# Kernel optimization log

Hardware: AMD Instinct MI355X
Metric: run time of the kernel (lower is better)

Reference implementation:

```python
import jax, jax.numpy as jnp
import numpy as np

B, H, N, D, RPE = 2, 8, 4096, 64, 64
LAYERS = 3


def _rms(x):
    # SimpleRMSNorm: x / sqrt(mean(x^2) + eps), no learned scale
    return x / jnp.sqrt(jnp.mean(x * x, axis=-1, keepdims=True) + 1e-8)


def setup_inputs() -> dict:
    key = jax.random.key(0)
    ks = jax.random.split(key, 7)
    s = 1.0 / np.sqrt(RPE)
    return {
        "x": jax.random.normal(ks[0], (B, H, N, D), dtype=jnp.float32),
        "w_in": jax.random.normal(ks[1], (1, RPE), dtype=jnp.float32) * 0.5,
        "b_in": jax.random.normal(ks[2], (RPE,), dtype=jnp.float32) * 0.02,
        "w_hid": jax.random.normal(ks[3], (LAYERS, RPE, RPE), dtype=jnp.float32) * s,
        "b_hid": jax.random.normal(ks[4], (LAYERS, RPE), dtype=jnp.float32) * 0.02,
        "w_out": jax.random.normal(ks[5], (RPE, H * D), dtype=jnp.float32) * s,
        "b_out": jax.random.normal(ks[6], (H * D,), dtype=jnp.float32) * 0.02,
    }


def reference(x, w_in, b_in, w_hid, b_hid, w_out, b_out):
    n = x.shape[-2]
    dt = x.dtype

    def rpe(idx):  # idx: (m, 1) relative-position features
        h = idx @ w_in + b_in  # (m, RPE)
        for i in range(LAYERS):  # non-residual: x = layer(x)
            h = jax.nn.relu(_rms(h)) @ w_hid[i] + b_hid[i]
        h = jax.nn.relu(_rms(h)) @ w_out + b_out  # (m, H*D)
        return h.reshape(-1, H, D).transpose(1, 0, 2)  # (H, m, D)

    zero_idx = jnp.ones((1, 1), dt)
    pos_idx = (1.0 / jnp.arange(2, n + 1, dtype=dt)).reshape(n - 1, 1)
    neg_idx = (-1.0 / jnp.arange(n, 1, -1, dtype=dt)).reshape(n - 1, 1)

    zero_k = rpe(zero_idx)  # (H, 1, D); used for both T[0] slots like the torch code
    a = jnp.concatenate([zero_k, rpe(pos_idx), zero_k, rpe(neg_idx)], axis=1)  # (H, 2n, D)
    # act_type='none' -> identity activation on a

    # Toeplitz matvec as circular conv of length 2n via FFT
    y = jnp.fft.rfft(x, 2 * n, axis=-2)          # (B, H, n+1, D) complex
    v = jnp.fft.rfft(a, 2 * n, axis=-2)[None]    # (1, H, n+1, D) complex
    out = jnp.fft.irfft(v * y, 2 * n, axis=-2)[:, :, :n, :]
    return out.astype(dt)
```

## Files before the change

kernel.cpp:

```cpp
#include <hip/hip_runtime.h>

#define N_SEQ 4096
#define N_FFT 8192
#define LAYERS 3
#define FT 512
#define PIDX(i) ((i) + ((i) >> 5))

template<int M>
__device__ inline void pass16_fwd(float* re, float* im, int tid)
{
    const int Q = M >> 4;
    const int j = tid & (Q - 1);
    const int G = tid / Q;
    const int base = G * M + j;
    const float KR[4] = {1.f, 0.9238795325f, 0.7071067812f, 0.3826834324f};
    const float KI[4] = {0.f, -0.3826834324f, -0.7071067812f, -0.9238795325f};
    float xr[4][4], xi[4][4];
#pragma unroll
    for (int a = 0; a < 4; ++a)
#pragma unroll
        for (int b = 0; b < 4; ++b) {
            int idx = PIDX(base + a * (M >> 2) + b * Q);
            xr[a][b] = re[idx]; xi[a][b] = im[idx];
        }
    float cj, sj;
    __sincosf(-6.283185307179586f / (float)M * (float)j, &sj, &cj);
#pragma unroll
    for (int b = 0; b < 4; ++b) {
        float c1 = cj * KR[b] - sj * KI[b];
        float s1 = cj * KI[b] + sj * KR[b];
        float c2 = c1 * c1 - s1 * s1, s2 = 2.f * c1 * s1;
        float c3 = c2 * c1 - s2 * s1, s3 = c2 * s1 + s2 * c1;
        float ar = xr[0][b] + xr[2][b], ai = xi[0][b] + xi[2][b];
        float br = xr[0][b] - xr[2][b], bi = xi[0][b] - xi[2][b];
        float cr = xr[1][b] + xr[3][b], ci = xi[1][b] + xi[3][b];
        float dr = xi[1][b] - xi[3][b], di = -(xr[1][b] - xr[3][b]);
        xr[0][b] = ar + cr;               xi[0][b] = ai + ci;
        float t1r = br + dr, t1i = bi + di;
        xr[1][b] = t1r * c1 - t1i * s1;   xi[1][b] = t1r * s1 + t1i * c1;
        float t2r = ar - cr, t2i = ai - ci;
        xr[2][b] = t2r * c2 - t2i * s2;   xi[2][b] = t2r * s2 + t2i * c2;
        float t3r = br - dr, t3i = bi - di;
        xr[3][b] = t3r * c3 - t3i * s3;   xi[3][b] = t3r * s3 + t3i * c3;
    }
    {
        float e1c = cj * cj - sj * sj, e1s = 2.f * cj * sj;
        float c1 = e1c * e1c - e1s * e1s, s1 = 2.f * e1c * e1s;
        float c2 = c1 * c1 - s1 * s1, s2 = 2.f * c1 * s1;
        float c3 = c2 * c1 - s2 * s1, s3 = c2 * s1 + s2 * c1;
#pragma unroll
        for (int a = 0; a < 4; ++a) {
            float ar = xr[a][0] + xr[a][2], ai = xi[a][0] + xi[a][2];
            float br = xr[a][0] - xr[a][2], bi = xi[a][0] - xi[a][2];
            float cr = xr[a][1] + xr[a][3], ci = xi[a][1] + xi[a][3];
            float dr = xi[a][1] - xi[a][3], di = -(xr[a][1] - xr[a][3]);
            xr[a][0] = ar + cr;               xi[a][0] = ai + ci;
            float t1r = br + dr, t1i = bi + di;
            xr[a][1] = t1r * c1 - t1i * s1;   xi[a][1] = t1r * s1 + t1i * c1;
            float t2r = ar - cr, t2i = ai - ci;
            xr[a][2] = t2r * c2 - t2i * s2;   xi[a][2] = t2r * s2 + t2i * c2;
            float t3r = br - dr, t3i = bi - di;
            xr[a][3] = t3r * c3 - t3i * s3;   xi[a][3] = t3r * s3 + t3i * c3;
        }
    }
#pragma unroll
    for (int a = 0; a < 4; ++a)
#pragma unroll
        for (int b = 0; b < 4; ++b) {
            int idx = PIDX(base + a * (M >> 2) + b * Q);
            re[idx] = xr[a][b]; im[idx] = xi[a][b];
        }
}

template<int M>
__device__ inline void pass16_inv(float* re, float* im, int tid)
{
    const int Q = M >> 4;
    const int j = tid & (Q - 1);
    const int G = tid / Q;
    const int base = G * M + j;
    const float KR[4] = {1.f, 0.9238795325f, 0.7071067812f, 0.3826834324f};
    const float KI[4] = {0.f, 0.3826834324f, 0.7071067812f, 0.9238795325f};
    float xr[4][4], xi[4][4];
#pragma unroll
    for (int a = 0; a < 4; ++a)
#pragma unroll
        for (int b = 0; b < 4; ++b) {
            int idx = PIDX(base + a * (M >> 2) + b * Q);
            xr[a][b] = re[idx]; xi[a][b] = im[idx];
        }
    float cj, sj;
    __sincosf(6.283185307179586f / (float)M * (float)j, &sj, &cj);
    {
        float e1c = cj * cj - sj * sj, e1s = 2.f * cj * sj;
        float c1 = e1c * e1c - e1s * e1s, s1 = 2.f * e1c * e1s;
        float c2 = c1 * c1 - s1 * s1, s2 = 2.f * c1 * s1;
        float c3 = c2 * c1 - s2 * s1, s3 = c2 * s1 + s2 * c1;
#pragma unroll
        for (int a = 0; a < 4; ++a) {
            float t0r = xr[a][0], t0i = xi[a][0];
            float t1r = xr[a][1] * c1 - xi[a][1] * s1, t1i = xr[a][1] * s1 + xi[a][1] * c1;
            float t2r = xr[a][2] * c2 - xi[a][2] * s2, t2i = xr[a][2] * s2 + xi[a][2] * c2;
            float t3r = xr[a][3] * c3 - xi[a][3] * s3, t3i = xr[a][3] * s3 + xi[a][3] * c3;
            float pr = t0r + t2r, pi = t0i + t2i;
            float qr = t0r - t2r, qi = t0i - t2i;
            float rr = t1r + t3r, ri = t1i + t3i;
            float sr = -(t1i - t3i), si = t1r - t3r;
            xr[a][0] = pr + rr; xi[a][0] = pi + ri;
            xr[a][1] = qr + sr; xi[a][1] = qi + si;
            xr[a][2] = pr - rr; xi[a][2] = pi - ri;
            xr[a][3] = qr - sr; xi[a][3] = qi - si;
        }
    }
#pragma unroll
    for (int b = 0; b < 4; ++b) {
        float c1 = cj * KR[b] - sj * KI[b];
        float s1 = cj * KI[b] + sj * KR[b];
        float c2 = c1 * c1 - s1 * s1, s2 = 2.f * c1 * s1;
        float c3 = c2 * c1 - s2 * s1, s3 = c2 * s1 + s2 * c1;
        float t0r = xr[0][b], t0i = xi[0][b];
        float t1r = xr[1][b] * c1 - xi[1][b] * s1, t1i = xr[1][b] * s1 + xi[1][b] * c1;
        float t2r = xr[2][b] * c2 - xi[2][b] * s2, t2i = xr[2][b] * s2 + xi[2][b] * c2;
        float t3r = xr[3][b] * c3 - xi[3][b] * s3, t3i = xr[3][b] * s3 + xi[3][b] * c3;
        float pr = t0r + t2r, pi = t0i + t2i;
        float qr = t0r - t2r, qi = t0i - t2i;
        float rr = t1r + t3r, ri = t1i + t3i;
        float sr = -(t1i - t3i), si = t1r - t3r;
        xr[0][b] = pr + rr; xi[0][b] = pi + ri;
        xr[1][b] = qr + sr; xi[1][b] = qi + si;
        xr[2][b] = pr - rr; xi[2][b] = pi - ri;
        xr[3][b] = qr - sr; xi[3][b] = qi - si;
    }
#pragma unroll
    for (int a = 0; a < 4; ++a)
#pragma unroll
        for (int b = 0; b < 4; ++b) {
            int idx = PIDX(base + a * (M >> 2) + b * Q);
            re[idx] = xr[a][b]; im[idx] = xi[a][b];
        }
}

__device__ inline void fwd8(float* zr, float* zi, int o)
{
    const float R = 0.70710678118654752f;
    {
        float ar = zr[o] + zr[o+4], ai = zi[o] + zi[o+4];
        float br = zr[o] - zr[o+4], bi = zi[o] - zi[o+4];
        float cr = zr[o+2] + zr[o+6], ci = zi[o+2] + zi[o+6];
        float dr = zi[o+2] - zi[o+6], di = -(zr[o+2] - zr[o+6]);
        zr[o]   = ar + cr; zi[o]   = ai + ci;
        zr[o+2] = br + dr; zi[o+2] = bi + di;
        zr[o+4] = ar - cr; zi[o+4] = ai - ci;
        zr[o+6] = br - dr; zi[o+6] = bi - di;
    }
    {
        float ar = zr[o+1] + zr[o+5], ai = zi[o+1] + zi[o+5];
        float br = zr[o+1] - zr[o+5], bi = zi[o+1] - zi[o+5];
        float cr = zr[o+3] + zr[o+7], ci = zi[o+3] + zi[o+7];
        float dr = zi[o+3] - zi[o+7], di = -(zr[o+3] - zr[o+7]);
        zr[o+1] = ar + cr; zi[o+1] = ai + ci;
        float t1r = br + dr, t1i = bi + di;
        zr[o+3] = R * (t1r + t1i); zi[o+3] = R * (t1i - t1r);
        float t2r = ar - cr, t2i = ai - ci;
        zr[o+5] = t2i;  zi[o+5] = -t2r;
        float t3r = br - dr, t3i = bi - di;
        zr[o+7] = R * (t3i - t3r); zi[o+7] = -R * (t3r + t3i);
    }
#pragma unroll
    for (int p = 0; p < 8; p += 2) {
        float ur = zr[o+p], ui = zi[o+p], vr = zr[o+p+1], vi = zi[o+p+1];
        zr[o+p]   = ur + vr; zi[o+p]   = ui + vi;
        zr[o+p+1] = ur - vr; zi[o+p+1] = ui - vi;
    }
}

__device__ inline void inv8(float* zr, float* zi, int o)
{
    const float R = 0.70710678118654752f;
#pragma unroll
    for (int p = 0; p < 8; p += 2) {
        float ur = zr[o+p], ui = zi[o+p], vr = zr[o+p+1], vi = zi[o+p+1];
        zr[o+p]   = ur + vr; zi[o+p]   = ui + vi;
        zr[o+p+1] = ur - vr; zi[o+p+1] = ui - vi;
    }
    {
        float t0r = zr[o],   t0i = zi[o];
        float t1r = zr[o+2], t1i = zi[o+2];
        float t2r = zr[o+4], t2i = zi[o+4];
        float t3r = zr[o+6], t3i = zi[o+6];
        float pr = t0r + t2r, pi = t0i + t2i;
        float qr = t0r - t2r, qi = t0i - t2i;
        float rr = t1r + t3r, ri = t1i + t3i;
        float sr = -(t1i - t3i), si = t1r - t3r;
        zr[o]   = pr + rr; zi[o]   = pi + ri;
        zr[o+2] = qr + sr; zi[o+2] = qi + si;
        zr[o+4] = pr - rr; zi[o+4] = pi - ri;
        zr[o+6] = qr - sr; zi[o+6] = qi - si;
    }
    {
        float t0r = zr[o+1], t0i = zi[o+1];
        float yr = zr[o+3], yi = zi[o+3];
        float t1r = R * (yr - yi), t1i = R * (yr + yi);
        yr = zr[o+5]; yi = zi[o+5];
        float t2r = -yi, t2i = yr;
        yr = zr[o+7]; yi = zi[o+7];
        float t3r = -R * (yr + yi), t3i = R * (yr - yi);
        float pr = t0r + t2r, pi = t0i + t2i;
        float qr = t0r - t2r, qi = t0i - t2i;
        float rr = t1r + t3r, ri = t1i + t3i;
        float sr = -(t1i - t3i), si = t1r - t3r;
        zr[o+1] = pr + rr; zi[o+1] = pi + ri;
        zr[o+3] = qr + sr; zi[o+3] = qi + si;
        zr[o+5] = pr - rr; zi[o+5] = pi - ri;
        zr[o+7] = qr - sr; zi[o+7] = qi - si;
    }
}

__global__ __launch_bounds__(256) void prep_kernel(
    const float* __restrict__ x,
    const float* __restrict__ w_in, const float* __restrict__ b_in,
    const float* __restrict__ w_hid, const float* __restrict__ b_hid,
    const float* __restrict__ w_out, const float* __restrict__ b_out,
    float* __restrict__ a_t, float2* __restrict__ xt2)
{
    __shared__ __align__(16) char smem[33536];
    const int tid = threadIdx.x;

    if (blockIdx.x >= 256) {
        float (*t0)[65] = (float (*)[65])smem;
        float (*t1)[65] = (float (*)[65])(smem + 16640);
        int bb = blockIdx.x - 256;
        int h = bb >> 6;
        int nb = bb & 63;
        int lx = tid & 63;
        int ly = tid >> 6;
        const float* s0 = x + ((size_t)h * N_SEQ + nb * 64) * 64;
        const float* s1 = x + ((size_t)(8 + h) * N_SEQ + nb * 64) * 64;
        for (int r = ly; r < 64; r += 4) {
            t0[r][lx] = s0[r * 64 + lx];
            t1[r][lx] = s1[r * 64 + lx];
        }
        __syncthreads();
        for (int r = ly; r < 64; r += 4) {
            float2* dst = xt2 + (size_t)(h * 64 + r) * N_SEQ + nb * 64;
            dst[lx] = make_float2(t0[lx][r], t1[lx][r]);
        }
        return;
    }

    float4* wl       = (float4*)smem;
    float (*ubuf)[65] = (float (*)[65])(smem + 16384);
    float (*sums)[9]  = (float (*)[9])(smem + 24704);
    const int p   = tid & 31;
    const int oct = tid >> 5;
    const int pos = blockIdx.x * 32 + p;

    float v;
    if (pos == 0 || pos == N_SEQ) v = 1.0f;
    else if (pos < N_SEQ)         v = 1.0f / (float)(pos + 1);
    else                          v = -1.0f / (float)(2 * N_SEQ + 1 - pos);

    float h[8];
#pragma unroll
    for (int i = 0; i < 8; ++i) {
        int f = oct * 8 + i;
        h[i] = v * w_in[f] + b_in[f];
    }
    for (int L = 0; L < LAYERS; ++L) {
        const float4* wsrc = (const float4*)(w_hid + L * 4096);
#pragma unroll
        for (int i = 0; i < 4; ++i) wl[i * 256 + tid] = wsrc[i * 256 + tid];
        float s = 0.f;
#pragma unroll
        for (int i = 0; i < 8; ++i) s += h[i] * h[i];
        sums[p][oct] = s;
        __syncthreads();
        float tot = 0.f;
#pragma unroll
        for (int g = 0; g < 8; ++g) tot += sums[p][g];
        float r = rsqrtf(tot * (1.f / 64.f) + 1e-8f);
#pragma unroll
        for (int i = 0; i < 8; ++i)
            ubuf[p][oct * 8 + i] = fmaxf(h[i] * r, 0.f);
        __syncthreads();
        float acc[8];
#pragma unroll
        for (int i = 0; i < 8; ++i) acc[i] = b_hid[L * 64 + oct * 8 + i];
#pragma unroll 4
        for (int j = 0; j < 64; ++j) {
            float uj = ubuf[p][j];
            float4 w0 = wl[j * 16 + oct * 2];
            float4 w1 = wl[j * 16 + oct * 2 + 1];
            acc[0] = fmaf(uj, w0.x, acc[0]); acc[1] = fmaf(uj, w0.y, acc[1]);
            acc[2] = fmaf(uj, w0.z, acc[2]); acc[3] = fmaf(uj, w0.w, acc[3]);
            acc[4] = fmaf(uj, w1.x, acc[4]); acc[5] = fmaf(uj, w1.y, acc[5]);
            acc[6] = fmaf(uj, w1.z, acc[6]); acc[7] = fmaf(uj, w1.w, acc[7]);
        }
#pragma unroll
        for (int i = 0; i < 8; ++i) h[i] = acc[i];
        __syncthreads();
    }
    {
        float s = 0.f;
#pragma unroll
        for (int i = 0; i < 8; ++i) s += h[i] * h[i];
        sums[p][oct] = s;
        __syncthreads();
        float tot = 0.f;
#pragma unroll
        for (int g = 0; g < 8; ++g) tot += sums[p][g];
        float r = rsqrtf(tot * (1.f / 64.f) + 1e-8f);
#pragma unroll
        for (int i = 0; i < 8; ++i)
            ubuf[p][oct * 8 + i] = fmaxf(h[i] * r, 0.f);
        __syncthreads();
    }
    for (int c = 0; c < 8; ++c) {
        float4 wreg[4];
#pragma unroll
        for (int cc = 0; cc < 4; ++cc) {
            int i4 = cc * 256 + tid;
            int j = i4 >> 4, q = i4 & 15;
            wreg[cc] = *(const float4*)(w_out + j * 512 + c * 64 + q * 4);
        }
        __syncthreads();
#pragma unroll
        for (int cc = 0; cc < 4; ++cc) wl[cc * 256 + tid] = wreg[cc];
        __syncthreads();
        float acc[8];
#pragma unroll
        for (int i = 0; i < 8; ++i) acc[i] = b_out[c * 64 + oct * 8 + i];
#pragma unroll 4
        for (int j = 0; j < 64; ++j) {
            float uj = ubuf[p][j];
            float4 w0 = wl[j * 16 + oct * 2];
            float4 w1 = wl[j * 16 + oct * 2 + 1];
            acc[0] = fmaf(uj, w0.x, acc[0]); acc[1] = fmaf(uj, w0.y, acc[1]);
            acc[2] = fmaf(uj, w0.z, acc[2]); acc[3] = fmaf(uj, w0.w, acc[3]);
            acc[4] = fmaf(uj, w1.x, acc[4]); acc[5] = fmaf(uj, w1.y, acc[5]);
            acc[6] = fmaf(uj, w1.z, acc[6]); acc[7] = fmaf(uj, w1.w, acc[7]);
        }
#pragma unroll
        for (int i = 0; i < 8; ++i)
            a_t[(size_t)(c * 64 + oct * 8 + i) * N_FFT + pos] = acc[i];
    }
}

__global__ __launch_bounds__(FT, 4) void conv_kernel(const float* __restrict__ a_t,
                                                     const float2* __restrict__ xt2,
                                                     float2* __restrict__ out_t2)
{
    __shared__ float re[8448];
    __shared__ float im[8448];
    const int tid = threadIdx.x;
    const int hd = blockIdx.x;
    const float JR = 0.9238795325f;
    const float JI = -0.3826834324f;

    {
        const float* src = a_t + (size_t)hd * N_FFT;
        float ck, sk;
        __sincosf(-6.283185307179586f / 8192.f * (float)tid, &sk, &ck);
#pragma unroll
        for (int pp = 0; pp < 4; ++pp) {
            int k = pp * FT + tid;
            float x0 = src[k], x1 = src[k + 2048], x2 = src[k + 4096], x3 = src[k + 6144];
            float ar = x0 + x2, br = x0 - x2;
            float cr = x1 + x3, e = x1 - x3;
            re[PIDX(k)] = ar + cr; im[PIDX(k)] = 0.f;
            float c1 = ck, s1 = sk;
            float c2 = c1 * c1 - s1 * s1, s2 = 2.f * c1 * s1;
            float c3 = c2 * c1 - s2 * s1, s3 = c2 * s1 + s2 * c1;
            re[PIDX(k + 2048)] = br * c1 + e * s1;  im[PIDX(k + 2048)] = br * s1 - e * c1;
            float t2r = ar - cr;
            re[PIDX(k + 4096)] = t2r * c2;          im[PIDX(k + 4096)] = t2r * s2;
            re[PIDX(k + 6144)] = br * c3 - e * s3;  im[PIDX(k + 6144)] = br * s3 + e * c3;
            float tc = ck * JR - sk * JI; sk = ck * JI + sk * JR; ck = tc;
        }
    }
    __syncthreads();
    pass16_fwd<2048>(re, im, tid);
    __syncthreads();
    pass16_fwd<128>(re, im, tid);
    __syncthreads();
    float afr[16], afi[16];
    {
        const int base = tid * 16;
        float zr[16], zi[16];
#pragma unroll
        for (int c = 0; c < 16; ++c) { int idx = PIDX(base + c); zr[c] = re[idx]; zi[c] = im[idx]; }
        fwd8(zr, zi, 0); fwd8(zr, zi, 8);
        const float inv = 1.0f / (float)N_FFT;
#pragma unroll
        for (int c = 0; c < 16; ++c) { afr[c] = zr[c] * inv; afi[c] = zi[c] * inv; }
    }
    __syncthreads();
    {
        const float2* src = xt2 + (size_t)hd * N_SEQ;
        float ck, sk;
        __sincosf(-6.283185307179586f / 8192.f * (float)tid, &sk, &ck);
#pragma unroll
        for (int pp = 0; pp < 4; ++pp) {
            int k = pp * FT + tid;
            float2 z0 = src[k], z1 = src[k + 2048];
            float ar = z0.x, ai = z0.y;
            float cr = z1.x, ci = z1.y;
            float dr = z1.y, di = -z1.x;
            re[PIDX(k)] = ar + cr; im[PIDX(k)] = ai + ci;
            float c1 = ck, s1 = sk;
            float c2 = c1 * c1 - s1 * s1, s2 = 2.f * c1 * s1;
            float c3 = c2 * c1 - s2 * s1, s3 = c2 * s1 + s2 * c1;
            float t1r = ar + dr, t1i = ai + di;
            re[PIDX(k + 2048)] = t1r * c1 - t1i * s1; im[PIDX(k + 2048)] = t1r * s1 + t1i * c1;
            float t2r = ar - cr, t2i = ai - ci;
            re[PIDX(k + 4096)] = t2r * c2 - t2i * s2; im[PIDX(k + 4096)] = t2r * s2 + t2i * c2;
            float t3r = ar - dr, t3i = ai - di;
            re[PIDX(k + 6144)] = t3r * c3 - t3i * s3; im[PIDX(k + 6144)] = t3r * s3 + t3i * c3;
            float tc = ck * JR - sk * JI; sk = ck * JI + sk * JR; ck = tc;
        }
    }
    __syncthreads();
    pass16_fwd<2048>(re, im, tid);
    __syncthreads();
    pass16_fwd<128>(re, im, tid);
    __syncthreads();
    {
        const int base = tid * 16;
        float zr[16], zi[16];
#pragma unroll
        for (int c = 0; c < 16; ++c) { int idx = PIDX(base + c); zr[c] = re[idx]; zi[c] = im[idx]; }
        fwd8(zr, zi, 0); fwd8(zr, zi, 8);
#pragma unroll
        for (int c = 0; c < 16; ++c) {
            float xr = zr[c], xi_ = zi[c];
            zr[c] = xr * afr[c] - xi_ * afi[c];
            zi[c] = xr * afi[c] + xi_ * afr[c];
        }
        inv8(zr, zi, 0); inv8(zr, zi, 8);
#pragma unroll
        for (int c = 0; c < 16; ++c) { int idx = PIDX(base + c); re[idx] = zr[c]; im[idx] = zi[c]; }
    }
    __syncthreads();
    pass16_inv<128>(re, im, tid);
    __syncthreads();
    pass16_inv<2048>(re, im, tid);
    __syncthreads();
    {
        float2* dst = out_t2 + (size_t)hd * N_SEQ;
        float ck, sk;
        __sincosf(6.283185307179586f / 8192.f * (float)tid, &sk, &ck);
        const float JcR = 0.9238795325f, JcI = 0.3826834324f;
#pragma unroll
        for (int pp = 0; pp < 4; ++pp) {
            int k = pp * FT + tid;
            float c1 = ck, s1 = sk;
            float c2 = c1 * c1 - s1 * s1, s2 = 2.f * c1 * s1;
            float c3 = c2 * c1 - s2 * s1, s3 = c2 * s1 + s2 * c1;
            float t0r = re[PIDX(k)],        t0i = im[PIDX(k)];
            float y1r = re[PIDX(k + 2048)], y1i = im[PIDX(k + 2048)];
            float y2r = re[PIDX(k + 4096)], y2i = im[PIDX(k + 4096)];
            float y3r = re[PIDX(k + 6144)], y3i = im[PIDX(k + 6144)];
            float t1r = y1r * c1 - y1i * s1, t1i = y1r * s1 + y1i * c1;
            float t2r = y2r * c2 - y2i * s2, t2i = y2r * s2 + y2i * c2;
            float t3r = y3r * c3 - y3i * s3, t3i = y3r * s3 + y3i * c3;
            float pr = t0r + t2r, pi = t0i + t2i;
            float qr = t0r - t2r, qi = t0i - t2i;
            float rr = t1r + t3r, ri = t1i + t3i;
            float sr = -(t1i - t3i), si = t1r - t3r;
            dst[k]        = make_float2(pr + rr, pi + ri);
            dst[k + 2048] = make_float2(qr + sr, qi + si);
            float tc = ck * JcR - sk * JcI; sk = ck * JcI + sk * JcR; ck = tc;
        }
    }
}

__global__ __launch_bounds__(256) void transpose_o_kernel(const float2* __restrict__ out_t2,
                                                          float* __restrict__ out)
{
    __shared__ float t0[64][65];
    __shared__ float t1[64][65];
    int h = blockIdx.x >> 6;
    int nb = blockIdx.x & 63;
    int lx = threadIdx.x & 63;
    int ly = threadIdx.x >> 6;
    for (int r = ly; r < 64; r += 4) {
        float2 v = out_t2[(size_t)(h * 64 + r) * N_SEQ + nb * 64 + lx];
        t0[r][lx] = v.x;
        t1[r][lx] = v.y;
    }
    __syncthreads();
    float* d0 = out + ((size_t)h * N_SEQ + nb * 64) * 64;
    float* d1 = out + ((size_t)(8 + h) * N_SEQ + nb * 64) * 64;
    for (int r = ly; r < 64; r += 4) {
        d0[r * 64 + lx] = t0[lx][r];
        d1[r * 64 + lx] = t1[lx][r];
    }
}

extern "C" void kernel_launch(void* const* d_in, const int* in_sizes, int n_in,
                              void* d_out, int out_size, void* d_ws, size_t ws_size,
                              hipStream_t stream)
{
    const float* x     = (const float*)d_in[0];
    const float* w_in  = (const float*)d_in[1];
    const float* b_in  = (const float*)d_in[2];
    const float* w_hid = (const float*)d_in[3];
    const float* b_hid = (const float*)d_in[4];
    const float* w_out = (const float*)d_in[5];
    const float* b_out = (const float*)d_in[6];
    float* out = (float*)d_out;

    char* ws = (char*)d_ws;
    float2* xt2    = (float2*)ws;
    float*  a_t    = (float*)(ws + (size_t)16 * 1024 * 1024);
    float2* out_t2 = (float2*)(ws + (size_t)32 * 1024 * 1024);

    prep_kernel<<<768, 256, 0, stream>>>(x, w_in, b_in, w_hid, b_hid, w_out, b_out,
                                         a_t, xt2);
    conv_kernel<<<512, FT, 0, stream>>>(a_t, xt2, out_t2);
    transpose_o_kernel<<<512, 256, 0, stream>>>(out_t2, out);
}
```

Before: 169.7 us.

## Widen prep blocks to 512 threads, relax conv launch bounds, defer FFT scaling

The prep kernel now runs 512-thread blocks handling 64 positions each, halving the MLP block count and loading each weight tile with fewer, wider per-thread copies. The transpose blocks use 8 row groups per pass. The conv kernel's launch bounds drop from 4 to 2 blocks per SM to give the compiler more registers, and the 1/N scale moves from the kernel-spectrum setup into the pointwise product. The relaxed bound may cost occupancy, and the larger MLP blocks reduce parallelism across the grid.

```diff
diff --git a/kernel.cpp b/kernel.cpp
--- a/kernel.cpp
+++ b/kernel.cpp
@@ -216,44 +216,44 @@
     }
 }
 
-__global__ __launch_bounds__(256) void prep_kernel(
+__global__ __launch_bounds__(512) void prep_kernel(
     const float* __restrict__ x,
     const float* __restrict__ w_in, const float* __restrict__ b_in,
     const float* __restrict__ w_hid, const float* __restrict__ b_hid,
     const float* __restrict__ w_out, const float* __restrict__ b_out,
     float* __restrict__ a_t, float2* __restrict__ xt2)
 {
-    __shared__ __align__(16) char smem[33536];
+    __shared__ __align__(16) char smem[35328];
     const int tid = threadIdx.x;
 
-    if (blockIdx.x >= 256) {
+    if (blockIdx.x >= 128) {
         float (*t0)[65] = (float (*)[65])smem;
         float (*t1)[65] = (float (*)[65])(smem + 16640);
-        int bb = blockIdx.x - 256;
+        int bb = blockIdx.x - 128;
         int h = bb >> 6;
         int nb = bb & 63;
         int lx = tid & 63;
         int ly = tid >> 6;
         const float* s0 = x + ((size_t)h * N_SEQ + nb * 64) * 64;
         const float* s1 = x + ((size_t)(8 + h) * N_SEQ + nb * 64) * 64;
-        for (int r = ly; r < 64; r += 4) {
+        for (int r = ly; r < 64; r += 8) {
             t0[r][lx] = s0[r * 64 + lx];
             t1[r][lx] = s1[r * 64 + lx];
         }
         __syncthreads();
-        for (int r = ly; r < 64; r += 4) {
+        for (int r = ly; r < 64; r += 8) {
             float2* dst = xt2 + (size_t)(h * 64 + r) * N_SEQ + nb * 64;
             dst[lx] = make_float2(t0[lx][r], t1[lx][r]);
         }
         return;
     }
 
-    float4* wl       = (float4*)smem;
+    float4* wl        = (float4*)smem;
     float (*ubuf)[65] = (float (*)[65])(smem + 16384);
-    float (*sums)[9]  = (float (*)[9])(smem + 24704);
-    const int p   = tid & 31;
-    const int oct = tid >> 5;
-    const int pos = blockIdx.x * 32 + p;
+    float (*sums)[9]  = (float (*)[9])(smem + 33024);
+    const int p   = tid & 63;
+    const int oct = tid >> 6;
+    const int pos = blockIdx.x * 64 + p;
 
     float v;
     if (pos == 0 || pos == N_SEQ) v = 1.0f;
@@ -268,8 +268,8 @@
     }
     for (int L = 0; L < LAYERS; ++L) {
         const float4* wsrc = (const float4*)(w_hid + L * 4096);
-#pragma unroll
-        for (int i = 0; i < 4; ++i) wl[i * 256 + tid] = wsrc[i * 256 + tid];
+        wl[tid] = wsrc[tid];
+        wl[tid + 512] = wsrc[tid + 512];
         float s = 0.f;
 #pragma unroll
         for (int i = 0; i < 8; ++i) s += h[i] * h[i];
@@ -316,16 +316,16 @@
         __syncthreads();
     }
     for (int c = 0; c < 8; ++c) {
-        float4 wreg[4];
-#pragma unroll
-        for (int cc = 0; cc < 4; ++cc) {
-            int i4 = cc * 256 + tid;
-            int j = i4 >> 4, q = i4 & 15;
-            wreg[cc] = *(const float4*)(w_out + j * 512 + c * 64 + q * 4);
-        }
-        __syncthreads();
-#pragma unroll
-        for (int cc = 0; cc < 4; ++cc) wl[cc * 256 + tid] = wreg[cc];
+        float4 wreg0, wreg1;
+        {
+            int i4 = tid;
+            wreg0 = *(const float4*)(w_out + (i4 >> 4) * 512 + c * 64 + (i4 & 15) * 4);
+            i4 = tid + 512;
+            wreg1 = *(const float4*)(w_out + (i4 >> 4) * 512 + c * 64 + (i4 & 15) * 4);
+        }
+        __syncthreads();
+        wl[tid] = wreg0;
+        wl[tid + 512] = wreg1;
         __syncthreads();
         float acc[8];
 #pragma unroll
@@ -346,7 +346,7 @@
     }
 }
 
-__global__ __launch_bounds__(FT, 4) void conv_kernel(const float* __restrict__ a_t,
+__global__ __launch_bounds__(FT, 2) void conv_kernel(const float* __restrict__ a_t,
                                                      const float2* __restrict__ xt2,
                                                      float2* __restrict__ out_t2)
 {
@@ -386,13 +386,9 @@
     float afr[16], afi[16];
     {
         const int base = tid * 16;
-        float zr[16], zi[16];
-#pragma unroll
-        for (int c = 0; c < 16; ++c) { int idx = PIDX(base + c); zr[c] = re[idx]; zi[c] = im[idx]; }
-        fwd8(zr, zi, 0); fwd8(zr, zi, 8);
-        const float inv = 1.0f / (float)N_FFT;
-#pragma unroll
-        for (int c = 0; c < 16; ++c) { afr[c] = zr[c] * inv; afi[c] = zi[c] * inv; }
+#pragma unroll
+        for (int c = 0; c < 16; ++c) { int idx = PIDX(base + c); afr[c] = re[idx]; afi[c] = im[idx]; }
+        fwd8(afr, afi, 0); fwd8(afr, afi, 8);
     }
     __syncthreads();
     {
@@ -430,11 +426,12 @@
 #pragma unroll
         for (int c = 0; c < 16; ++c) { int idx = PIDX(base + c); zr[c] = re[idx]; zi[c] = im[idx]; }
         fwd8(zr, zi, 0); fwd8(zr, zi, 8);
+        const float inv = 1.0f / (float)N_FFT;
 #pragma unroll
         for (int c = 0; c < 16; ++c) {
             float xr = zr[c], xi_ = zi[c];
-            zr[c] = xr * afr[c] - xi_ * afi[c];
-            zi[c] = xr * afi[c] + xi_ * afr[c];
+            zr[c] = (xr * afr[c] - xi_ * afi[c]) * inv;
+            zi[c] = (xr * afi[c] + xi_ * afr[c]) * inv;
         }
         inv8(zr, zi, 0); inv8(zr, zi, 8);
 #pragma unroll
@@ -515,7 +512,7 @@
     float*  a_t    = (float*)(ws + (size_t)16 * 1024 * 1024);
     float2* out_t2 = (float2*)(ws + (size_t)32 * 1024 * 1024);
 
-    prep_kernel<<<768, 256, 0, stream>>>(x, w_in, b_in, w_hid, b_hid, w_out, b_out,
+    prep_kernel<<<640, 512, 0, stream>>>(x, w_in, b_in, w_hid, b_hid, w_out, b_out,
                                          a_t, xt2);
     conv_kernel<<<512, FT, 0, stream>>>(a_t, xt2, out_t2);
     transpose_o_kernel<<<512, 256, 0, stream>>>(out_t2, out);
```

Result: faster. 151.1 us (-11.0%).
